# Optimization experiments

Hardware: AMD Instinct MI355X
Metric: run time of the kernel (lower is better)

The kernel has to match this reference:

```python
import jax, jax.numpy as jnp
import numpy as np

BETA = 0.25

def setup_inputs() -> dict:
    key = jax.random.key(0)
    k1, k2 = jax.random.split(key)
    z = jax.random.normal(k1, (32, 64, 64, 64), dtype=jnp.float32)  # (B, D, H, W)
    # EmbeddingEMA init: uniform(-1/K, 1/K)
    K, D = 1024, 64
    weight = jax.random.uniform(k2, (K, D), dtype=jnp.float32, minval=-1.0 / K, maxval=1.0 / K)
    return {"z": z, "weight": weight}


def reference(z, weight):
    b, d, h, w = z.shape
    K = weight.shape[0]
    # permute (B,D,H,W) -> (B,H,W,D) and flatten to (N, D)
    z_flat = jnp.transpose(z, (0, 2, 3, 1)).reshape(-1, d)
    # squared euclidean distance: ||z||^2 + ||c||^2 - 2 z c^T  -> (N, K)
    distance = (
        jnp.sum(z_flat * z_flat, axis=1, keepdims=True)
        + jnp.sum(weight * weight, axis=1)
        - 2.0 * jnp.matmul(z_flat, weight.T)
    )
    vq_indices = jnp.argmin(distance, axis=1)  # (N,)
    z_quantized = weight[vq_indices]  # gather (N, D)
    # one-hot scatter stats (training-time EMA inputs)
    vq_current_count = jax.ops.segment_sum(
        jnp.ones((z_flat.shape[0],), dtype=z_flat.dtype), vq_indices, num_segments=K)
    vq_current_sum = jax.ops.segment_sum(z_flat, vq_indices, num_segments=K)  # (K, D)
    commitment_loss = jnp.mean((z_flat - jax.lax.stop_gradient(z_quantized)) ** 2)
    loss = BETA * commitment_loss
    # straight-through estimator
    q = z_flat + jax.lax.stop_gradient(z_quantized - z_flat)
    q = jnp.transpose(q.reshape(b, h, w, d), (0, 3, 1, 2))  # back to (B, D, H, W)
    return q, loss, commitment_loss, vq_current_count, vq_current_sum
```

## Files before the change

### kernel.cpp

```cpp
#include <hip/hip_runtime.h>


#define HWsz   4096
#define Dd     64
#define Kk     1024
#define NB     32
#define NTOT   131072
#define QSIZE  (NTOT * Dd)
#define BETA_C 0.25f
#define DIST_BLOCKS 1024

typedef float  f32x16 __attribute__((ext_vector_type(16)));
typedef short  bf16x8 __attribute__((ext_vector_type(8)));

#define MF32(a, b, c) __builtin_amdgcn_mfma_f32_32x32x16_bf16((a), (b), (c), 0, 0, 0)

__device__ __forceinline__ unsigned short f2bf(float f) {
    unsigned u = __float_as_uint(f);
    u += 0x7FFF + ((u >> 16) & 1);
    return (unsigned short)(u >> 16);
}
__device__ __forceinline__ float bf2f(unsigned short b) {
    return __uint_as_float(((unsigned)b) << 16);
}

__global__ __launch_bounds__(256) void vq_prep(const float* __restrict__ w,
                                               float* __restrict__ c2,
                                               unsigned short* __restrict__ whi,
                                               unsigned short* __restrict__ wlo) {
    int t = blockIdx.x * 256 + threadIdx.x;
    int k = t >> 6, d = t & 63;
    float v = w[t];
    unsigned short hb = f2bf(v);
    unsigned short lb = f2bf(v - bf2f(hb));
    int ct = k >> 5, col = k & 31;
    int s = d >> 4, half = (d >> 3) & 1, j = d & 7;
    int lane = half * 32 + col;
    int idx = (((ct * 4 + s) * 64) + lane) * 8 + j;
    whi[idx] = hb; wlo[idx] = lb;

    if (t < Kk) {
        const float4* c4 = reinterpret_cast<const float4*>(w + t * Dd);
        float s0 = 0.f, s1 = 0.f, s2 = 0.f, s3 = 0.f;
#pragma unroll
        for (int q = 0; q < 16; ++q) {
            float4 cq = c4[q];
            s0 = fmaf(cq.x, cq.x, s0); s1 = fmaf(cq.y, cq.y, s1);
            s2 = fmaf(cq.z, cq.z, s2); s3 = fmaf(cq.w, cq.w, s3);
        }
        c2[t] = (s0 + s1) + (s2 + s3);
    }
}

__global__ __launch_bounds__(256) void vq_dist(const float* __restrict__ z,
                                               const float* __restrict__ w,
                                               const float* __restrict__ c2,
                                               const unsigned short* __restrict__ whi,
                                               const unsigned short* __restrict__ wlo,
                                               float* __restrict__ out,
                                               float* __restrict__ commit_ws,
                                               int* __restrict__ idx_ws) {
    const int lane = threadIdx.x & 63;
    const int wid  = threadIdx.x >> 6;
    const int b    = blockIdx.x >> 5;
    const int hwb  = (blockIdx.x & 31) * 128 + wid * 32;
    const int c32  = lane & 31;
    const int dh   = (lane >> 5) * 8;

    const float* zbase = z + (size_t)b * (Dd * HWsz) + hwb + c32;
    bf16x8 zhi[4], zlo[4];
#pragma unroll
    for (int s = 0; s < 4; ++s) {
        bf16x8 h, l;
#pragma unroll
        for (int j = 0; j < 8; ++j) {
            float zz = zbase[(size_t)(16 * s + dh + j) * HWsz];
            unsigned short hb = f2bf(zz);
            unsigned short lb = f2bf(zz - bf2f(hb));
            h[j] = (short)hb; l[j] = (short)lb;
        }
        zhi[s] = h; zlo[s] = l;
    }

    float best[16];
    int   bk[16];
#pragma unroll
    for (int r = 0; r < 16; ++r) { best[r] = 3.4e38f; bk[r] = 0; }

    const bf16x8* pha = reinterpret_cast<const bf16x8*>(whi) + lane;
    const bf16x8* pla = reinterpret_cast<const bf16x8*>(wlo) + lane;
    const bf16x8* phb = pha + 256;
    const bf16x8* plb = pla + 256;
    const float*  cvp = c2 + c32;

#define LOADB(H0, H1, H2, H3, L0, L1, L2, L3, CV, PH, PL, CTI)   \
    {                                                            \
        H0 = (PH)[0 * 64]; H1 = (PH)[1 * 64];                    \
        H2 = (PH)[2 * 64]; H3 = (PH)[3 * 64];                    \
        L0 = (PL)[0 * 64]; L1 = (PL)[1 * 64];                    \
        L2 = (PL)[2 * 64]; L3 = (PL)[3 * 64];                    \
        CV = cvp[(CTI) * 32];                                    \
    }

#define COMPUTE(H0, H1, H2, H3, L0, L1, L2, L3, CV, CT)                        \
    {                                                                          \
        f32x16 p = {0.f,0.f,0.f,0.f,0.f,0.f,0.f,0.f,0.f,0.f,0.f,0.f,0.f,0.f,0.f,0.f}; \
        f32x16 q = {0.f,0.f,0.f,0.f,0.f,0.f,0.f,0.f,0.f,0.f,0.f,0.f,0.f,0.f,0.f,0.f}; \
        p = MF32(zhi[0], H0, p);  q = MF32(zhi[2], H2, q);                     \
        p = MF32(zhi[1], H1, p);  q = MF32(zhi[3], H3, q);                     \
        p = MF32(zlo[0], H0, p);  q = MF32(zlo[2], H2, q);                     \
        p = MF32(zlo[1], H1, p);  q = MF32(zlo[3], H3, q);                     \
        p = MF32(zhi[0], L0, p);  q = MF32(zhi[2], L2, q);                     \
        p = MF32(zhi[1], L1, p);  q = MF32(zhi[3], L3, q);                     \
        const int kc = (CT) * 32 + c32;                                        \
        _Pragma("unroll")                                                      \
        for (int r = 0; r < 16; ++r) {                                         \
            float sc = fmaf(-2.f, p[r] + q[r], CV);                            \
            if (sc < best[r]) { best[r] = sc; bk[r] = kc; }                    \
        }                                                                      \
    }

    bf16x8 aH0, aH1, aH2, aH3, aL0, aL1, aL2, aL3;
    bf16x8 bH0, bH1, bH2, bH3, bL0, bL1, bL2, bL3;
    float  acv, bcv;

    LOADB(aH0, aH1, aH2, aH3, aL0, aL1, aL2, aL3, acv, pha, pla, 0);

    for (int it = 0; it < 16; ++it) {
        const int ct = it * 2;
        LOADB(bH0, bH1, bH2, bH3, bL0, bL1, bL2, bL3, bcv, phb, plb, ct + 1);
        COMPUTE(aH0, aH1, aH2, aH3, aL0, aL1, aL2, aL3, acv, ct);
        pha += 512; pla += 512;
        if (it < 15)
            LOADB(aH0, aH1, aH2, aH3, aL0, aL1, aL2, aL3, acv, pha, pla, ct + 2);
        COMPUTE(bH0, bH1, bH2, bH3, bL0, bL1, bL2, bL3, bcv, ct + 1);
        phb += 512; plb += 512;
    }

#pragma unroll
    for (int off = 1; off < 32; off <<= 1) {
#pragma unroll
        for (int r = 0; r < 16; ++r) {
            float ob = __shfl_xor(best[r], off, 64);
            int   ok = __shfl_xor(bk[r],   off, 64);
            if (ob < best[r] || (ob == best[r] && ok < bk[r])) {
                best[r] = ob; bk[r] = ok;
            }
        }
    }

    const int hi5   = ((lane >> 2) & 1) << 5;
    const int myreg = (lane & 3) + (((lane >> 3) & 3) << 2);
    int mybk = 0;
#pragma unroll
    for (int re = 0; re < 16; ++re) {
        int t = __shfl(bk[re], hi5, 64);
        if (re == myreg) mybk = t;
    }

    if (lane < 32) idx_ws[(size_t)b * HWsz + hwb + lane] = mybk;

    float* qbase = out + (size_t)b * (Dd * HWsz) + hwb + c32;
    float commit = 0.f;
#pragma unroll
    for (int s = 0; s < 4; ++s) {
        const float4* cw = reinterpret_cast<const float4*>(w + mybk * Dd + 16 * s + dh);
        float4 p0 = cw[0], p1 = cw[1];
        float cbv[8] = {p0.x, p0.y, p0.z, p0.w, p1.x, p1.y, p1.z, p1.w};
#pragma unroll
        for (int j = 0; j < 8; ++j) {
            int   d  = 16 * s + dh + j;
            float zz = bf2f((unsigned short)zhi[s][j]) + bf2f((unsigned short)zlo[s][j]);
            float cc = cbv[j];
            qbase[(size_t)d * HWsz] = zz + (cc - zz);
            float dd = zz - cc;
            commit = fmaf(dd, dd, commit);
        }
    }

#pragma unroll
    for (int off = 32; off > 0; off >>= 1) commit += __shfl_down(commit, off, 64);

    __shared__ float red[4];
    if (lane == 0) red[wid] = commit;
    __syncthreads();
    if (threadIdx.x == 0)
        commit_ws[blockIdx.x] = (red[0] + red[1]) + (red[2] + red[3]);
}

__global__ __launch_bounds__(256) void vq_stats(const float* __restrict__ z,
                                                const int* __restrict__ idx_ws,
                                                float* __restrict__ psum,
                                                float* __restrict__ pcnt) {
    const int b  = blockIdx.x >> 5;
    const int dp = blockIdx.x & 31;
    const int d0 = dp * 2;
    const bool docnt = (dp == 0);

    __shared__ float acc0[Kk], acc1[Kk], cnt[Kk];
    for (int i = threadIdx.x; i < Kk; i += 256) { acc0[i] = 0.f; acc1[i] = 0.f; cnt[i] = 0.f; }
    __syncthreads();

    const int4*   ip  = reinterpret_cast<const int4*>(idx_ws + (size_t)b * HWsz);
    const float4* zp0 = reinterpret_cast<const float4*>(z + ((size_t)b * Dd + d0) * HWsz);
    const float4* zp1 = reinterpret_cast<const float4*>(z + ((size_t)b * Dd + d0 + 1) * HWsz);
#pragma unroll
    for (int it = 0; it < 4; ++it) {
        int c4 = it * 256 + threadIdx.x;
        int4   k4 = ip[c4];
        float4 v0 = zp0[c4];
        float4 v1 = zp1[c4];
        atomicAdd(&acc0[k4.x], v0.x); atomicAdd(&acc0[k4.y], v0.y);
        atomicAdd(&acc0[k4.z], v0.z); atomicAdd(&acc0[k4.w], v0.w);
        atomicAdd(&acc1[k4.x], v1.x); atomicAdd(&acc1[k4.y], v1.y);
        atomicAdd(&acc1[k4.z], v1.z); atomicAdd(&acc1[k4.w], v1.w);
        if (docnt) {
            atomicAdd(&cnt[k4.x], 1.f); atomicAdd(&cnt[k4.y], 1.f);
            atomicAdd(&cnt[k4.z], 1.f); atomicAdd(&cnt[k4.w], 1.f);
        }
    }
    __syncthreads();

    float* po = psum + ((size_t)b * Dd + d0) * Kk;
    for (int i = threadIdx.x; i < Kk; i += 256) { po[i] = acc0[i]; po[Kk + i] = acc1[i]; }
    if (docnt) {
        float* pc = pcnt + (size_t)b * Kk;
        for (int i = threadIdx.x; i < Kk; i += 256) pc[i] = cnt[i];
    }
}

__global__ __launch_bounds__(256) void vq_reduce(const float* __restrict__ psum,
                                                 const float* __restrict__ pcnt,
                                                 const float* __restrict__ commit_ws,
                                                 float* __restrict__ out) {
    int t = blockIdx.x * 256 + threadIdx.x;
    int k = t & 1023, d = t >> 10;
    float s = 0.f;
#pragma unroll
    for (int b = 0; b < NB; ++b)
        s += psum[((size_t)b * Dd + d) * Kk + k];
    out[QSIZE + 2 + Kk + (size_t)k * Dd + d] = s;
    if (t < Kk) {
        float c = 0.f;
#pragma unroll
        for (int b = 0; b < NB; ++b) c += pcnt[((size_t)b << 10) + t];
        out[QSIZE + 2 + t] = c;
    }

    if (blockIdx.x == 0) {
        float cs = 0.f;
        for (int i = threadIdx.x; i < DIST_BLOCKS; i += 256) cs += commit_ws[i];
#pragma unroll
        for (int off = 32; off > 0; off >>= 1) cs += __shfl_down(cs, off, 64);
        __shared__ float r2[4];
        const int lane = threadIdx.x & 63, wid = threadIdx.x >> 6;
        if (lane == 0) r2[wid] = cs;
        __syncthreads();
        if (threadIdx.x == 0) {
            float c = ((r2[0] + r2[1]) + (r2[2] + r2[3])) / (float)QSIZE;
            out[QSIZE]     = BETA_C * c;
            out[QSIZE + 1] = c;
        }
    }
}

extern "C" void kernel_launch(void* const* d_in, const int* in_sizes, int n_in,
                              void* d_out, int out_size, void* d_ws, size_t ws_size,
                              hipStream_t stream) {
    const float* z = (const float*)d_in[0];
    const float* w = (const float*)d_in[1];
    float* out = (float*)d_out;

    float* commit_ws = (float*)d_ws;
    float* c2        = (float*)d_ws + 1024;
    unsigned short* whi = (unsigned short*)((float*)d_ws + 2048);
    unsigned short* wlo = whi + (Kk * Dd);
    int*   idx_ws = (int*)(wlo + (Kk * Dd));
    float* pcnt   = (float*)(idx_ws + NTOT);
    float* psum   = pcnt + (size_t)NB * Kk;

    vq_prep<<<(Kk * Dd) / 256, 256, 0, stream>>>(w, c2, whi, wlo);
    vq_dist<<<DIST_BLOCKS, 256, 0, stream>>>(z, w, c2, whi, wlo, out, commit_ws, idx_ws);
    vq_stats<<<NB * 32, 256, 0, stream>>>(z, idx_ws, psum, pcnt);
    vq_reduce<<<(Kk * Dd) / 256, 256, 0, stream>>>(psum, pcnt, commit_ws, out);
}
```

Before: 243.9 us.

## Restructure distance kernel: codebook-stationary waves, LDS-staged z tiles, split-K argmin families

The distance kernel is reorganised so each wave keeps one 32-code codebook tile in registers while z rows stream through double-buffered, swizzled LDS tiles. The codebook is split into four families whose partial argmax results go to workspace, and a new epilogue kernel merges them and does the gather, output write and commitment loss. The -0.5*||c||^2 bias is folded into an extra MFMA via an augmented bf16 column. This removes the per-wave reload of the whole codebook and moves the bias into the matrix unit, at the cost of an extra kernel, workspace traffic for the partial results, and reading z twice. Rounding ||c||^2 to bf16 and using only a hi part may change argmin ties or near-ties.

```diff
diff --git a/kernel.cpp b/kernel.cpp
--- a/kernel.cpp
+++ b/kernel.cpp
@@ -8,181 +8,226 @@
 #define NTOT   131072
 #define QSIZE  (NTOT * Dd)
 #define BETA_C 0.25f
-#define DIST_BLOCKS 1024
+#define NFAM   4
+#define ROWS_PER_BLK 512
+#define NT     16
+#define EPI_BLOCKS 512
 
 typedef float  f32x16 __attribute__((ext_vector_type(16)));
 typedef short  bf16x8 __attribute__((ext_vector_type(8)));
+typedef unsigned short ushort_t;
+typedef unsigned long long u64;
 
 #define MF32(a, b, c) __builtin_amdgcn_mfma_f32_32x32x16_bf16((a), (b), (c), 0, 0, 0)
 
-__device__ __forceinline__ unsigned short f2bf(float f) {
+__device__ __forceinline__ ushort_t f2bf(float f) {
     unsigned u = __float_as_uint(f);
     u += 0x7FFF + ((u >> 16) & 1);
-    return (unsigned short)(u >> 16);
-}
-__device__ __forceinline__ float bf2f(unsigned short b) {
+    return (ushort_t)(u >> 16);
+}
+__device__ __forceinline__ float bf2f(ushort_t b) {
     return __uint_as_float(((unsigned)b) << 16);
 }
+__device__ __forceinline__ u64 pack4(ushort_t a, ushort_t b, ushort_t c, ushort_t d) {
+    return (u64)a | ((u64)b << 16) | ((u64)c << 32) | ((u64)d << 48);
+}
 
 __global__ __launch_bounds__(256) void vq_prep(const float* __restrict__ w,
-                                               float* __restrict__ c2,
-                                               unsigned short* __restrict__ whi,
-                                               unsigned short* __restrict__ wlo) {
+                                               ushort_t* __restrict__ whi,
+                                               ushort_t* __restrict__ wlo) {
     int t = blockIdx.x * 256 + threadIdx.x;
-    int k = t >> 6, d = t & 63;
-    float v = w[t];
-    unsigned short hb = f2bf(v);
-    unsigned short lb = f2bf(v - bf2f(hb));
-    int ct = k >> 5, col = k & 31;
-    int s = d >> 4, half = (d >> 3) & 1, j = d & 7;
-    int lane = half * 32 + col;
-    int idx = (((ct * 4 + s) * 64) + lane) * 8 + j;
-    whi[idx] = hb; wlo[idx] = lb;
-
-    if (t < Kk) {
-        const float4* c4 = reinterpret_cast<const float4*>(w + t * Dd);
-        float s0 = 0.f, s1 = 0.f, s2 = 0.f, s3 = 0.f;
-#pragma unroll
-        for (int q = 0; q < 16; ++q) {
-            float4 cq = c4[q];
-            s0 = fmaf(cq.x, cq.x, s0); s1 = fmaf(cq.y, cq.y, s1);
-            s2 = fmaf(cq.z, cq.z, s2); s3 = fmaf(cq.w, cq.w, s3);
-        }
-        c2[t] = (s0 + s1) + (s2 + s3);
-    }
-}
-
-__global__ __launch_bounds__(256) void vq_dist(const float* __restrict__ z,
-                                               const float* __restrict__ w,
-                                               const float* __restrict__ c2,
-                                               const unsigned short* __restrict__ whi,
-                                               const unsigned short* __restrict__ wlo,
-                                               float* __restrict__ out,
-                                               float* __restrict__ commit_ws,
-                                               int* __restrict__ idx_ws) {
-    const int lane = threadIdx.x & 63;
-    const int wid  = threadIdx.x >> 6;
-    const int b    = blockIdx.x >> 5;
-    const int hwb  = (blockIdx.x & 31) * 128 + wid * 32;
-    const int c32  = lane & 31;
-    const int dh   = (lane >> 5) * 8;
-
-    const float* zbase = z + (size_t)b * (Dd * HWsz) + hwb + c32;
-    bf16x8 zhi[4], zlo[4];
-#pragma unroll
-    for (int s = 0; s < 4; ++s) {
-        bf16x8 h, l;
-#pragma unroll
-        for (int j = 0; j < 8; ++j) {
-            float zz = zbase[(size_t)(16 * s + dh + j) * HWsz];
-            unsigned short hb = f2bf(zz);
-            unsigned short lb = f2bf(zz - bf2f(hb));
-            h[j] = (short)hb; l[j] = (short)lb;
-        }
-        zhi[s] = h; zlo[s] = l;
-    }
-
-    float best[16];
-    int   bk[16];
-#pragma unroll
-    for (int r = 0; r < 16; ++r) { best[r] = 3.4e38f; bk[r] = 0; }
-
-    const bf16x8* pha = reinterpret_cast<const bf16x8*>(whi) + lane;
-    const bf16x8* pla = reinterpret_cast<const bf16x8*>(wlo) + lane;
-    const bf16x8* phb = pha + 256;
-    const bf16x8* plb = pla + 256;
-    const float*  cvp = c2 + c32;
-
-#define LOADB(H0, H1, H2, H3, L0, L1, L2, L3, CV, PH, PL, CTI)   \
-    {                                                            \
-        H0 = (PH)[0 * 64]; H1 = (PH)[1 * 64];                    \
-        H2 = (PH)[2 * 64]; H3 = (PH)[3 * 64];                    \
-        L0 = (PL)[0 * 64]; L1 = (PL)[1 * 64];                    \
-        L2 = (PL)[2 * 64]; L3 = (PL)[3 * 64];                    \
-        CV = cvp[(CTI) * 32];                                    \
-    }
-
-#define COMPUTE(H0, H1, H2, H3, L0, L1, L2, L3, CV, CT)                        \
-    {                                                                          \
-        f32x16 p = {0.f,0.f,0.f,0.f,0.f,0.f,0.f,0.f,0.f,0.f,0.f,0.f,0.f,0.f,0.f,0.f}; \
-        f32x16 q = {0.f,0.f,0.f,0.f,0.f,0.f,0.f,0.f,0.f,0.f,0.f,0.f,0.f,0.f,0.f,0.f}; \
-        p = MF32(zhi[0], H0, p);  q = MF32(zhi[2], H2, q);                     \
-        p = MF32(zhi[1], H1, p);  q = MF32(zhi[3], H3, q);                     \
-        p = MF32(zlo[0], H0, p);  q = MF32(zlo[2], H2, q);                     \
-        p = MF32(zlo[1], H1, p);  q = MF32(zlo[3], H3, q);                     \
-        p = MF32(zhi[0], L0, p);  q = MF32(zhi[2], L2, q);                     \
-        p = MF32(zhi[1], L1, p);  q = MF32(zhi[3], L3, q);                     \
-        const int kc = (CT) * 32 + c32;                                        \
-        _Pragma("unroll")                                                      \
-        for (int r = 0; r < 16; ++r) {                                         \
-            float sc = fmaf(-2.f, p[r] + q[r], CV);                            \
-            if (sc < best[r]) { best[r] = sc; bk[r] = kc; }                    \
-        }                                                                      \
-    }
-
-    bf16x8 aH0, aH1, aH2, aH3, aL0, aL1, aL2, aL3;
-    bf16x8 bH0, bH1, bH2, bH3, bL0, bL1, bL2, bL3;
-    float  acv, bcv;
-
-    LOADB(aH0, aH1, aH2, aH3, aL0, aL1, aL2, aL3, acv, pha, pla, 0);
-
-    for (int it = 0; it < 16; ++it) {
-        const int ct = it * 2;
-        LOADB(bH0, bH1, bH2, bH3, bL0, bL1, bL2, bL3, bcv, phb, plb, ct + 1);
-        COMPUTE(aH0, aH1, aH2, aH3, aL0, aL1, aL2, aL3, acv, ct);
-        pha += 512; pla += 512;
-        if (it < 15)
-            LOADB(aH0, aH1, aH2, aH3, aL0, aL1, aL2, aL3, acv, pha, pla, ct + 2);
-        COMPUTE(bH0, bH1, bH2, bH3, bL0, bL1, bL2, bL3, bcv, ct + 1);
-        phb += 512; plb += 512;
-    }
-
-#pragma unroll
-    for (int off = 1; off < 32; off <<= 1) {
-#pragma unroll
-        for (int r = 0; r < 16; ++r) {
-            float ob = __shfl_xor(best[r], off, 64);
-            int   ok = __shfl_xor(bk[r],   off, 64);
-            if (ob < best[r] || (ob == best[r] && ok < bk[r])) {
-                best[r] = ob; bk[r] = ok;
+    if (t < Kk * Dd) {
+        int k = t >> 6, d = t & 63;
+        float v = w[t];
+        ushort_t hb = f2bf(v);
+        ushort_t lb = f2bf(v - bf2f(hb));
+        int ct = k >> 5;
+        int s = d >> 4, h = (d >> 3) & 1, j = d & 7;
+        int lane = h * 32 + (k & 31);
+        int idx = (((ct * 5 + s) * 64) + lane) * 8 + j;
+        whi[idx] = hb; wlo[idx] = lb;
+    } else {
+        int u = t - Kk * Dd;
+        int ct = u >> 9, slot = u & 511;
+        int ln = slot >> 3, j = slot & 7;
+        ushort_t hb = 0;
+        if (ln < 32 && j == 0) {
+            const float4* c4 = reinterpret_cast<const float4*>(w + (ct * 32 + ln) * Dd);
+            float s0 = 0.f, s1 = 0.f, s2 = 0.f, s3 = 0.f;
+#pragma unroll
+            for (int q = 0; q < 16; ++q) {
+                float4 cq = c4[q];
+                s0 = fmaf(cq.x, cq.x, s0); s1 = fmaf(cq.y, cq.y, s1);
+                s2 = fmaf(cq.z, cq.z, s2); s3 = fmaf(cq.w, cq.w, s3);
             }
-        }
-    }
-
-    const int hi5   = ((lane >> 2) & 1) << 5;
-    const int myreg = (lane & 3) + (((lane >> 3) & 3) << 2);
-    int mybk = 0;
-#pragma unroll
-    for (int re = 0; re < 16; ++re) {
-        int t = __shfl(bk[re], hi5, 64);
-        if (re == myreg) mybk = t;
-    }
-
-    if (lane < 32) idx_ws[(size_t)b * HWsz + hwb + lane] = mybk;
-
-    float* qbase = out + (size_t)b * (Dd * HWsz) + hwb + c32;
+            hb = f2bf(-0.5f * ((s0 + s1) + (s2 + s3)));
+        }
+        int idx = (((ct * 5 + 4) * 64) + ln) * 8 + j;
+        whi[idx] = hb; wlo[idx] = 0;
+    }
+}
+
+__global__ __launch_bounds__(512) void vq_dist(const float* __restrict__ z,
+                                               const ushort_t* __restrict__ whi,
+                                               const ushort_t* __restrict__ wlo,
+                                               float* __restrict__ famS,
+                                               int* __restrict__ famK) {
+    const int tid  = threadIdx.x;
+    const int lane = tid & 63;
+    const int wid  = tid >> 6;
+    const int fam  = blockIdx.x >> 8;
+    const int rb   = blockIdx.x & 255;
+    const int b    = rb >> 3;
+    const int hw0  = (rb & 7) * ROWS_PER_BLK;
+    const int hi5  = lane >> 5;
+    const int ct   = fam * 8 + wid;
+    const int grp0 = ct * 32;
+
+    const bf16x8* PH = reinterpret_cast<const bf16x8*>(whi) + (size_t)(ct * 5) * 64 + lane;
+    const bf16x8* PL = reinterpret_cast<const bf16x8*>(wlo) + (size_t)(ct * 5) * 64 + lane;
+    bf16x8 ch0 = PH[0], ch1 = PH[64], ch2 = PH[128], ch3 = PH[192], cx = PH[256];
+    bf16x8 cl0 = PL[0], cl1 = PL[64], cl2 = PL[128], cl3 = PL[192];
+
+    bf16x8 zext = (bf16x8){0, 0, 0, 0, 0, 0, 0, 0};
+    if (lane < 32) zext[0] = (short)0x3F80;
+
+    __shared__ ushort_t zbH[2][2048];
+    __shared__ ushort_t zbL[2][2048];
+    __shared__ float mrgS[2][8][32];
+    __shared__ int   mrgK[2][8][32];
+
+    const int srow = tid & 31;
+    const int d0   = (tid >> 5) * 4;
+    const int woff = ((srow * 128 + d0 * 2) ^ ((srow & 7) << 4));
+    const float* zsrc = z + ((size_t)(b * Dd + d0)) * HWsz + hw0 + srow;
+
+#define ISSUE(TT, R0, R1, R2, R3)                              \
+    { const float* p_ = zsrc + (TT) * 32;                      \
+      R0 = p_[0]; R1 = p_[HWsz]; R2 = p_[2 * HWsz]; R3 = p_[3 * HWsz]; }
+
+#define WRITEB(TT, R0, R1, R2, R3)                                          \
+    { ushort_t h0_ = f2bf(R0), h1_ = f2bf(R1), h2_ = f2bf(R2), h3_ = f2bf(R3); \
+      ushort_t l0_ = f2bf(R0 - bf2f(h0_)), l1_ = f2bf(R1 - bf2f(h1_));      \
+      ushort_t l2_ = f2bf(R2 - bf2f(h2_)), l3_ = f2bf(R3 - bf2f(h3_));      \
+      *(u64*)((char*)&zbH[(TT) & 1][0] + woff) = pack4(h0_, h1_, h2_, h3_); \
+      *(u64*)((char*)&zbL[(TT) & 1][0] + woff) = pack4(l0_, l1_, l2_, l3_); }
+
+    const int roBase = (lane & 31) * 128 + hi5 * 16;
+    const int roSwz  = ((lane & 31) & 7) << 4;
+
+    float Ra0, Ra1, Ra2, Ra3, Rb0, Rb1, Rb2, Rb3;
+
+    ISSUE(0, Ra0, Ra1, Ra2, Ra3);
+    WRITEB(0, Ra0, Ra1, Ra2, Ra3);
+    ISSUE(1, Rb0, Rb1, Rb2, Rb3);
+    __syncthreads();
+
+#pragma unroll 2
+    for (int t = 0; t < NT; ++t) {
+        const int cur = t & 1;
+        const bool even = (cur == 0);
+        if (t < NT - 2) {
+            if (even) { ISSUE(t + 2, Ra0, Ra1, Ra2, Ra3); }
+            else      { ISSUE(t + 2, Rb0, Rb1, Rb2, Rb3); }
+        }
+
+        const char* hp = (const char*)&zbH[cur][0];
+        const char* lp = (const char*)&zbL[cur][0];
+        bf16x8 zh0 = *(const bf16x8*)(hp + ((roBase +  0) ^ roSwz));
+        bf16x8 zh1 = *(const bf16x8*)(hp + ((roBase + 32) ^ roSwz));
+        bf16x8 zh2 = *(const bf16x8*)(hp + ((roBase + 64) ^ roSwz));
+        bf16x8 zh3 = *(const bf16x8*)(hp + ((roBase + 96) ^ roSwz));
+        bf16x8 zl0 = *(const bf16x8*)(lp + ((roBase +  0) ^ roSwz));
+        bf16x8 zl1 = *(const bf16x8*)(lp + ((roBase + 32) ^ roSwz));
+        bf16x8 zl2 = *(const bf16x8*)(lp + ((roBase + 64) ^ roSwz));
+        bf16x8 zl3 = *(const bf16x8*)(lp + ((roBase + 96) ^ roSwz));
+
+        f32x16 acc = {0.f,0.f,0.f,0.f,0.f,0.f,0.f,0.f,0.f,0.f,0.f,0.f,0.f,0.f,0.f,0.f};
+        acc = MF32(ch0, zh0, acc);  acc = MF32(ch0, zl0, acc);  acc = MF32(cl0, zh0, acc);
+        acc = MF32(ch1, zh1, acc);  acc = MF32(ch1, zl1, acc);  acc = MF32(cl1, zh1, acc);
+        acc = MF32(ch2, zh2, acc);  acc = MF32(ch2, zl2, acc);  acc = MF32(cl2, zh2, acc);
+        acc = MF32(ch3, zh3, acc);  acc = MF32(ch3, zl3, acc);  acc = MF32(cl3, zh3, acc);
+        acc = MF32(cx, zext, acc);
+
+        float bs = acc[0];
+        int   bkk = grp0 + 4 * hi5;
+#pragma unroll
+        for (int r = 1; r < 16; ++r) {
+            int cd = grp0 + (r & 3) + 8 * (r >> 2) + 4 * hi5;
+            if (acc[r] > bs) { bs = acc[r]; bkk = cd; }
+        }
+        float os = __shfl_xor(bs, 32, 64);
+        int   ok = __shfl_xor(bkk, 32, 64);
+        if (os > bs || (os == bs && ok < bkk)) { bs = os; bkk = ok; }
+        if (lane < 32) { mrgS[cur][wid][lane] = bs; mrgK[cur][wid][lane] = bkk; }
+
+        if (t < NT - 1) {
+            if (even) { WRITEB(t + 1, Rb0, Rb1, Rb2, Rb3); }
+            else      { WRITEB(t + 1, Ra0, Ra1, Ra2, Ra3); }
+        }
+        __syncthreads();
+
+        if (wid == 0 && lane < 32) {
+            float ms = mrgS[cur][0][lane];
+            int   mk = mrgK[cur][0][lane];
+#pragma unroll
+            for (int g = 1; g < 8; ++g) {
+                float gs = mrgS[cur][g][lane];
+                int   gk = mrgK[cur][g][lane];
+                if (gs > ms) { ms = gs; mk = gk; }
+            }
+            int row = b * HWsz + hw0 + t * 32 + lane;
+            famS[(size_t)fam * NTOT + row] = ms;
+            famK[(size_t)fam * NTOT + row] = mk;
+        }
+    }
+#undef ISSUE
+#undef WRITEB
+}
+
+__global__ __launch_bounds__(256) void vq_epi(const float* __restrict__ z,
+                                              const float* __restrict__ w,
+                                              const float* __restrict__ famS,
+                                              const int* __restrict__ famK,
+                                              float* __restrict__ out,
+                                              int* __restrict__ idx_ws,
+                                              float* __restrict__ commit_ws) {
+    const int row = blockIdx.x * 256 + threadIdx.x;
+    const int b = row >> 12, hw = row & 4095;
+
+    float bs = famS[row];
+    int   bkk = famK[row];
+#pragma unroll
+    for (int f = 1; f < NFAM; ++f) {
+        float s2 = famS[(size_t)f * NTOT + row];
+        int   k2 = famK[(size_t)f * NTOT + row];
+        if (s2 > bs) { bs = s2; bkk = k2; }
+    }
+    idx_ws[row] = bkk;
+
+    const float* zr = z + (size_t)b * (Dd * HWsz) + hw;
+    float* qr = out + (size_t)b * (Dd * HWsz) + hw;
+    const float4* cw = reinterpret_cast<const float4*>(w + (size_t)bkk * Dd);
     float commit = 0.f;
 #pragma unroll
-    for (int s = 0; s < 4; ++s) {
-        const float4* cw = reinterpret_cast<const float4*>(w + mybk * Dd + 16 * s + dh);
-        float4 p0 = cw[0], p1 = cw[1];
-        float cbv[8] = {p0.x, p0.y, p0.z, p0.w, p1.x, p1.y, p1.z, p1.w};
-#pragma unroll
-        for (int j = 0; j < 8; ++j) {
-            int   d  = 16 * s + dh + j;
-            float zz = bf2f((unsigned short)zhi[s][j]) + bf2f((unsigned short)zlo[s][j]);
-            float cc = cbv[j];
-            qbase[(size_t)d * HWsz] = zz + (cc - zz);
-            float dd = zz - cc;
+    for (int c4 = 0; c4 < 16; ++c4) {
+        float4 cc = cw[c4];
+        float cv[4] = {cc.x, cc.y, cc.z, cc.w};
+#pragma unroll
+        for (int i = 0; i < 4; ++i) {
+            int d = c4 * 4 + i;
+            float zz = zr[(size_t)d * HWsz];
+            qr[(size_t)d * HWsz] = zz + (cv[i] - zz);
+            float dd = zz - cv[i];
             commit = fmaf(dd, dd, commit);
         }
     }
 
 #pragma unroll
     for (int off = 32; off > 0; off >>= 1) commit += __shfl_down(commit, off, 64);
-
     __shared__ float red[4];
-    if (lane == 0) red[wid] = commit;
+    const int lane = threadIdx.x & 63, wv = threadIdx.x >> 6;
+    if (lane == 0) red[wv] = commit;
     __syncthreads();
     if (threadIdx.x == 0)
         commit_ws[blockIdx.x] = (red[0] + red[1]) + (red[2] + red[3]);
@@ -249,12 +294,12 @@
 
     if (blockIdx.x == 0) {
         float cs = 0.f;
-        for (int i = threadIdx.x; i < DIST_BLOCKS; i += 256) cs += commit_ws[i];
+        for (int i = threadIdx.x; i < EPI_BLOCKS; i += 256) cs += commit_ws[i];
 #pragma unroll
         for (int off = 32; off > 0; off >>= 1) cs += __shfl_down(cs, off, 64);
         __shared__ float r2[4];
-        const int lane = threadIdx.x & 63, wid = threadIdx.x >> 6;
-        if (lane == 0) r2[wid] = cs;
+        const int lane = threadIdx.x & 63, wv = threadIdx.x >> 6;
+        if (lane == 0) r2[wv] = cs;
         __syncthreads();
         if (threadIdx.x == 0) {
             float c = ((r2[0] + r2[1]) + (r2[2] + r2[3])) / (float)QSIZE;
@@ -272,15 +317,17 @@
     float* out = (float*)d_out;
 
     float* commit_ws = (float*)d_ws;
-    float* c2        = (float*)d_ws + 1024;
-    unsigned short* whi = (unsigned short*)((float*)d_ws + 2048);
-    unsigned short* wlo = whi + (Kk * Dd);
-    int*   idx_ws = (int*)(wlo + (Kk * Dd));
-    float* pcnt   = (float*)(idx_ws + NTOT);
-    float* psum   = pcnt + (size_t)NB * Kk;
-
-    vq_prep<<<(Kk * Dd) / 256, 256, 0, stream>>>(w, c2, whi, wlo);
-    vq_dist<<<DIST_BLOCKS, 256, 0, stream>>>(z, w, c2, whi, wlo, out, commit_ws, idx_ws);
+    float* famS      = (float*)d_ws + 1024;
+    int*   famK      = (int*)((float*)d_ws + 1024 + 524288);
+    ushort_t* whi    = (ushort_t*)((float*)d_ws + 1024 + 2 * 524288);
+    ushort_t* wlo    = whi + 81920;
+    int*   idx_ws    = (int*)(wlo + 81920);
+    float* pcnt      = (float*)(idx_ws + NTOT);
+    float* psum      = pcnt + (size_t)NB * Kk;
+
+    vq_prep<<<(Kk * Dd + 16384) / 256, 256, 0, stream>>>(w, whi, wlo);
+    vq_dist<<<NFAM * 256, 512, 0, stream>>>(z, whi, wlo, famS, famK);
+    vq_epi<<<EPI_BLOCKS, 256, 0, stream>>>(z, w, famS, famK, out, idx_ws, commit_ws);
     vq_stats<<<NB * 32, 256, 0, stream>>>(z, idx_ws, psum, pcnt);
     vq_reduce<<<(Kk * Dd) / 256, 256, 0, stream>>>(psum, pcnt, commit_ws, out);
 }
```

Measured after the change: 216.2 us. -11.4%, faster.
